# Kernel optimization log

Hardware: AMD Instinct MI355X
Metric: run time of the kernel (lower is better)

The kernel has to match this reference:

```python
import jax, jax.numpy as jnp
import numpy as np
import math

D_MODEL = 1024
NHEAD = 16
HEAD_DIM = D_MODEL // NHEAD
ROPE_BASE = 10000.0


def _rope(x):
    # x: [B, H, S, Dh]; rotate per the RoPE class (half-split variant)
    d = x.shape[-1]
    half = d // 2
    seq_len = x.shape[2]
    theta = 1.0 / (ROPE_BASE ** (jnp.arange(0, d, 2, dtype=jnp.float32) / d))  # [d/2]
    ang = jnp.arange(seq_len, dtype=jnp.float32)[:, None] * theta[None, :]      # [S, d/2]
    ang2 = jnp.concatenate([ang, ang], axis=-1)                                 # [S, d]
    cos_ = jnp.cos(ang2)[None, None, :, :]
    sin_ = jnp.sin(ang2)[None, None, :, :]
    neg_half = jnp.concatenate([-x[..., half:], x[..., :half]], axis=-1)
    return x * cos_ + neg_half * sin_


def setup_inputs() -> dict:
    key = jax.random.key(0)
    ks = jax.random.split(key, 10)
    B, S, D = 4, 2048, D_MODEL
    scale = 1.0 / math.sqrt(D)
    x = jax.random.normal(ks[0], (B, S, D), dtype=jnp.float32)
    Wq = jax.random.normal(ks[1], (D, D), dtype=jnp.float32) * scale
    bq = jnp.zeros((D,), dtype=jnp.float32)
    Wk = jax.random.normal(ks[2], (D, D), dtype=jnp.float32) * scale
    bk = jnp.zeros((D,), dtype=jnp.float32)
    Wv = jax.random.normal(ks[3], (D, D), dtype=jnp.float32) * scale
    bv = jnp.zeros((D,), dtype=jnp.float32)
    Wo = jax.random.normal(ks[4], (D, D), dtype=jnp.float32) * scale
    bo = jnp.zeros((D,), dtype=jnp.float32)
    # causal mask: mask==1 means masked (upper triangle)
    mask = jnp.triu(jnp.ones((S, S), dtype=jnp.int32), k=1)[None, None, :, :]
    return {"x": x, "Wq": Wq, "bq": bq, "Wk": Wk, "bk": bk,
            "Wv": Wv, "bv": bv, "Wo": Wo, "bo": bo, "mask": mask}


def reference(x, Wq, bq, Wk, bk, Wv, bv, Wo, bo, mask):
    B, S, D = x.shape
    H, Dh = NHEAD, HEAD_DIM

    def proj(W, b):
        y = jnp.einsum('bsd,ed->bse', x, W) + b  # torch Linear: x @ W.T + b
        return y.reshape(B, S, H, Dh).transpose(0, 2, 1, 3)  # [B,H,S,Dh]

    q = _rope(proj(Wq, bq))
    k = _rope(proj(Wk, bk))
    v = proj(Wv, bv)

    a = jnp.einsum('bhqd,bhkd->bhqk', q, k) / math.sqrt(Dh)  # [B,H,S,S]
    a = jnp.where(mask == 1, jnp.float32(-1e9), a)
    a = jax.nn.softmax(a, axis=-1)
    out = jnp.einsum('bhqk,bhkd->bhqd', a, v)                 # [B,H,S,Dh]
    out = out.transpose(0, 2, 1, 3).reshape(B, S, D)
    return jnp.einsum('bsd,ed->bse', out, Wo) + bo
```

## Files before the change

### kernel.cpp

```cpp
#include <hip/hip_runtime.h>
#include <stdint.h>

typedef unsigned short u16;
typedef __bf16 bf16x8 __attribute__((ext_vector_type(8)));
typedef __bf16 bf16x2 __attribute__((ext_vector_type(2)));
typedef float f32x4 __attribute__((ext_vector_type(4)));
typedef float f32x16 __attribute__((ext_vector_type(16)));

#define SEQ    2048
#define NHEAD  16
#define DH     64
#define DMODEL 1024
#define NBH    64

__device__ __forceinline__ u16 cvt1(float f){
  union { __bf16 h; u16 u; } c; c.h = (__bf16)f; return c.u;
}
__device__ __forceinline__ uint32_t cvt2(float a, float b){
  union { bf16x2 v; uint32_t u; } c; c.v = bf16x2{(__bf16)a, (__bf16)b}; return c.u;
}
__device__ __forceinline__ int swz(int row){ return (((row&7)^((row>>3)&7))<<4); }

#if __has_builtin(__builtin_amdgcn_exp2f)
__device__ __forceinline__ float EXP2(float x){ return __builtin_amdgcn_exp2f(x); }
#else
__device__ __forceinline__ float EXP2(float x){ return exp2f(x); }
#endif
__device__ __forceinline__ float max3f(float a, float b, float c){
  float r; asm("v_max3_f32 %0, %1, %2, %3" : "=v"(r) : "v"(a), "v"(b), "v"(c));
  return r;
}

typedef const __attribute__((address_space(1))) uint32_t* gas_t;
typedef __attribute__((address_space(3))) uint32_t* las_t;
__device__ __forceinline__ void async16(const void* g, void* l){
  __builtin_amdgcn_global_load_lds((gas_t)g, (las_t)l, 16, 0, 0);
}

__device__ __forceinline__ void vstore8(char* dst, uint2 a0, uint2 a1,
                                        uint2 b0, uint2 b1, int dc, int vpos){
  uint32_t pk[8];
  pk[0] = __builtin_amdgcn_perm(b0.x, a0.x, 0x05040100u);
  pk[1] = __builtin_amdgcn_perm(b0.x, a0.x, 0x07060302u);
  pk[2] = __builtin_amdgcn_perm(b0.y, a0.y, 0x05040100u);
  pk[3] = __builtin_amdgcn_perm(b0.y, a0.y, 0x07060302u);
  pk[4] = __builtin_amdgcn_perm(b1.x, a1.x, 0x05040100u);
  pk[5] = __builtin_amdgcn_perm(b1.x, a1.x, 0x07060302u);
  pk[6] = __builtin_amdgcn_perm(b1.y, a1.y, 0x05040100u);
  pk[7] = __builtin_amdgcn_perm(b1.y, a1.y, 0x07060302u);
#pragma unroll
  for (int e=0;e<8;e++){
    const int row = dc*8 + e;
    *(uint32_t*)(dst + ((row*128 + vpos*2) ^ swz(row))) = pk[e];
  }
}

__global__ void prep(const float* __restrict__ x,  const float* __restrict__ Wq,
                     const float* __restrict__ Wk, const float* __restrict__ Wv,
                     const float* __restrict__ Wo,
                     u16* __restrict__ xb, u16* __restrict__ wqkv,
                     u16* __restrict__ wob, float* __restrict__ tab)
{
  const int bid = blockIdx.x, tid = threadIdx.x;
  if (bid < 6144){
    const float* src; u16* dst; int lb;
    if      (bid < 4096){ src = x;  dst = xb;              lb = bid; }
    else if (bid < 4608){ src = Wq; dst = wqkv;            lb = bid-4096; }
    else if (bid < 5120){ src = Wk; dst = wqkv + 1048576;  lb = bid-4608; }
    else if (bid < 5632){ src = Wv; dst = wqkv + 2097152;  lb = bid-5120; }
    else                { src = Wo; dst = wob;             lb = bid-5632; }
    const size_t off = (size_t)lb*2048 + tid*8;
    float4 a = *(const float4*)(src+off);
    float4 b = *(const float4*)(src+off+4);
    bf16x8 o = { (__bf16)a.x,(__bf16)a.y,(__bf16)a.z,(__bf16)a.w,
                 (__bf16)b.x,(__bf16)b.y,(__bf16)b.z,(__bf16)b.w };
    *(bf16x8*)(dst+off) = o;
  } else {
    const int t = (bid-6144)*256 + tid;
    const int s = t >> 5, j = t & 31;
    double freq = exp(-(double)(2*j)/64.0*log(10000.0));
    double ang = (double)s*freq;
    tab[s*64 + 2*j]     = (float)cos(ang);
    tab[s*64 + 2*j + 1] = (float)sin(ang);
  }
}

template<int MODE>
__global__ __launch_bounds__(256, 2)
void gemm_bt(const u16* __restrict__ A, const u16* __restrict__ W,
             const float* __restrict__ b0, const float* __restrict__ b1,
             const float* __restrict__ b2, float* __restrict__ fout,
             u16* __restrict__ dq, u16* __restrict__ dk, u16* __restrict__ dv,
             const float* __restrict__ tab)
{
  __shared__ u16 Ab[2][128*64];
  __shared__ u16 Bb[2][128*64];
  const int tid = threadIdx.x;
  const int lane = tid & 63;
  const int w = tid >> 6, wr = w >> 1, wc = w & 1;
  const int id = blockIdx.x;
  const int bx = id >> 6;
  const int by = ((id & 7) << 3) | ((id >> 3) & 7);
  const int m0 = by * 128;
  const int n0 = bx * 128;
  const int c0 = lane & 15, g = lane >> 4;

  f32x4 acc[4][4] = {};

  const int srow = tid >> 3;
  const int gcol = (((tid & 7) ^ (srow & 7)) << 4);
  const char* ga = (const char*)A + (size_t)(m0 + srow)*2048 + gcol;
  const char* gb = (const char*)W + (size_t)(n0 + srow)*2048 + gcol;
  const int ldst = tid*16;

#define STAGE_G(buf, kbyte) do{ \
    _Pragma("unroll") \
    for (int k=0;k<4;k++){ \
      async16(ga + (kbyte) + k*32*2048, (char*)Ab[buf] + k*4096 + ldst); \
      async16(gb + (kbyte) + k*32*2048, (char*)Bb[buf] + k*4096 + ldst); \
    } \
  }while(0)

#define COMPUTE_G(buf) do{ \
    bf16x8 afr[2][4], bfr[2][4]; \
    _Pragma("unroll") \
    for (int kk=0;kk<2;kk++){ \
      _Pragma("unroll") \
      for (int i=0;i<4;i++){ \
        const int ra = wr*64 + i*16 + c0; \
        afr[kk][i] = *(const bf16x8*)((const char*)Ab[buf] + ra*128 + ((((kk*4+g) ^ (ra&7))) << 4)); \
        const int rb = wc*64 + i*16 + c0; \
        bfr[kk][i] = *(const bf16x8*)((const char*)Bb[buf] + rb*128 + ((((kk*4+g) ^ (rb&7))) << 4)); \
      } \
    } \
    __builtin_amdgcn_s_setprio(1); \
    _Pragma("unroll") \
    for (int kk=0;kk<2;kk++) \
      _Pragma("unroll") \
      for (int i=0;i<4;i++) \
        _Pragma("unroll") \
        for (int j=0;j<4;j++) \
          acc[i][j] = __builtin_amdgcn_mfma_f32_16x16x32_bf16(afr[kk][i], bfr[kk][j], acc[i][j], 0,0,0); \
    __builtin_amdgcn_s_setprio(0); \
  }while(0)

  STAGE_G(0, 0);
#pragma unroll 1
  for (int it = 0; it < 15; ++it) {
    const int cur = it & 1;
    STAGE_G(cur ^ 1, (it+1)*128);
    asm volatile("s_waitcnt vmcnt(8)" ::: "memory");
    __builtin_amdgcn_s_barrier();
    __builtin_amdgcn_sched_barrier(0);
    COMPUTE_G(cur);
    __builtin_amdgcn_s_barrier();
    __builtin_amdgcn_sched_barrier(0);
  }
  asm volatile("s_waitcnt vmcnt(0)" ::: "memory");
  __builtin_amdgcn_s_barrier();
  __builtin_amdgcn_sched_barrier(0);
  COMPUTE_G(1);
#undef STAGE_G
#undef COMPUTE_G

  const int nbase = n0 + wc*64;
  const int t = n0 >> 10;
  const float* bias = (MODE==1) ? b0 : (t==0) ? b0 : (t==1) ? b1 : b2;
  float bv4[4];
#pragma unroll
  for (int j=0;j<4;j++) bv4[j] = bias[(nbase & 1023) + j*16 + c0];

  if (MODE == 0) {
    u16* dst = (t==0) ? dq : (t==1) ? dk : dv;
    const float qs = (t==0) ? 0.18033688011f : 1.0f;
    const int h = (nbase >> 6) & (NHEAD-1);
#pragma unroll
    for (int i=0;i<4;i++){
      const int mbase = m0 + wr*64 + i*16 + g*4;
#pragma unroll
      for (int r=0;r<4;r++){
        const int mm = mbase + r;
        const int bb = mm >> 11, s = mm & (SEQ-1);
        const size_t rowbase = (((size_t)(bb*NHEAD + h))*SEQ + s)*DH;
        if (t < 2) {
#pragma unroll
          for (int j2=0;j2<2;j2++){
            const int dh = j2*16 + c0;
            const float xl = acc[i][j2][r]   + bv4[j2];
            const float xh = acc[i][j2+2][r] + bv4[j2+2];
            const float2 cs = *(const float2*)(tab + (size_t)s*64 + dh*2);
            dst[rowbase + dh]      = cvt1((xl*cs.x - xh*cs.y)*qs);
            dst[rowbase + dh + 32] = cvt1((xh*cs.x + xl*cs.y)*qs);
          }
        } else {
#pragma unroll
          for (int j=0;j<4;j++)
            dst[rowbase + j*16 + c0] = cvt1(acc[i][j][r] + bv4[j]);
        }
      }
    }
  } else {
#pragma unroll
    for (int i=0;i<4;i++){
      const int mbase = m0 + wr*64 + i*16 + g*4;
#pragma unroll
      for (int j=0;j<4;j++){
#pragma unroll
        for (int r=0;r<4;r++)
          fout[(size_t)(mbase + r) * DMODEL + nbase + j*16 + c0] = acc[i][j][r] + bv4[j];
      }
    }
  }
}

__global__ __launch_bounds__(256, 2)
void attn_fwd(const u16* __restrict__ Q, const u16* __restrict__ K,
              const u16* __restrict__ V, u16* __restrict__ O)
{
  __shared__ u16 Kb[2][64*64];
  __shared__ u16 Vt[2][64*64];
  const int bh = blockIdx.x;
  const int pair = blockIdx.y;
  const int tid = threadIdx.x, lane = tid & 63, w = tid >> 6;
  const int c31 = lane & 31, hi = lane >> 5;
  const size_t hb = (size_t)bh * SEQ * DH;
  const int b = bh >> 4, h = bh & 15;

  const int boff1 = tid*16;
  const int ksw1  = boff1 ^ swz(boff1 >> 7);
  const int boff2 = boff1 + 4096;
  const int ksw2  = boff2 ^ swz(boff2 >> 7);
  const int rp = tid >> 3, dc = tid & 7;
  const int kv0 = 2*rp;
  const int vpos = (kv0 & 0x33) | ((kv0 & 4) << 1) | ((kv0 & 8) >> 1);

#pragma unroll 1
  for (int half = 0; half < 2; half++){
    const int qt = half ? (15 - pair) : pair;
    const int qrow_base = qt*128 + w*32;
    const int jt_last  = 2*qt + 1;
    const int jt_end_w = 2*qt + (w>>1);
    const int q = qrow_base + c31;

    bf16x8 qf[4];
#pragma unroll
    for (int kc=0;kc<4;kc++)
      qf[kc] = *(const bf16x8*)(Q + hb + (size_t)q*DH + kc*16 + hi*8);

    f32x16 oacc0 = {}, oacc1 = {};
    float mrun = -3.0e38f, lrun = 0.f;

    uint2 pa0, pa1, pb0, pb1;

    {
      const u16* gv = V + hb;
      pa0 = *(const uint2*)(gv + (kv0  )*DH + dc*8);
      pa1 = *(const uint2*)(gv + (kv0  )*DH + dc*8 + 4);
      pb0 = *(const uint2*)(gv + (kv0+1)*DH + dc*8);
      pb1 = *(const uint2*)(gv + (kv0+1)*DH + dc*8 + 4);
      __builtin_amdgcn_sched_barrier(0);
      const char* gk = (const char*)(K + hb);
      async16(gk + ksw1, (char*)Kb[0] + boff1);
      async16(gk + ksw2, (char*)Kb[0] + boff2);
      vstore8((char*)Vt[0], pa0, pa1, pb0, pb1, dc, vpos);
    }
    __syncthreads();

    for (int jt = 0; jt <= jt_last; jt++){
      const int cur = jt & 1, nxt = cur ^ 1;
      const bool pre = (jt < jt_last);
      if (pre){
        const u16* gv = V + hb + (size_t)(jt+1)*64*DH;
        pa0 = *(const uint2*)(gv + (kv0  )*DH + dc*8);
        pa1 = *(const uint2*)(gv + (kv0  )*DH + dc*8 + 4);
        pb0 = *(const uint2*)(gv + (kv0+1)*DH + dc*8);
        pb1 = *(const uint2*)(gv + (kv0+1)*DH + dc*8 + 4);
        __builtin_amdgcn_sched_barrier(0);
        const char* gk = (const char*)(K + hb + (size_t)(jt+1)*64*DH);
        async16(gk + ksw1, (char*)Kb[nxt] + boff1);
        async16(gk + ksw2, (char*)Kb[nxt] + boff2);
      }

      if (jt <= jt_end_w){
        if (pre) asm volatile("s_waitcnt vmcnt(6)" ::: "memory");
        else     asm volatile("s_waitcnt vmcnt(0)" ::: "memory");
        f32x16 sT[2] = {};
#pragma unroll
        for (int kc=0;kc<4;kc++){
          const int col = (kc*16 + hi*8)*2;
          const int r0 = c31, r1 = 32 + c31;
          const bf16x8 kf0 = *(const bf16x8*)((const char*)Kb[cur] + ((r0*128 + col) ^ swz(r0)));
          const bf16x8 kf1 = *(const bf16x8*)((const char*)Kb[cur] + ((r1*128 + col) ^ swz(r1)));
          __builtin_amdgcn_s_setprio(1);
          sT[0] = __builtin_amdgcn_mfma_f32_32x32x16_bf16(kf0, qf[kc], sT[0], 0,0,0);
          sT[1] = __builtin_amdgcn_mfma_f32_32x32x16_bf16(kf1, qf[kc], sT[1], 0,0,0);
          __builtin_amdgcn_s_setprio(0);
        }
        if (jt == jt_end_w){
#pragma unroll
          for (int kvb=0;kvb<2;kvb++)
#pragma unroll
            for (int r=0;r<16;r++){
              const int kv = jt*64 + kvb*32 + (r&3) + 8*(r>>2) + 4*hi;
              sT[kvb][r] = (kv <= q) ? sT[kvb][r] : -3.0e38f;
            }
        }
        float mx0 = -3.0e38f, mx1 = -3.0e38f;
#pragma unroll
        for (int r=0;r<16;r+=2){
          mx0 = max3f(mx0, sT[0][r], sT[0][r+1]);
          mx1 = max3f(mx1, sT[1][r], sT[1][r+1]);
        }
        float mx = fmaxf(mx0, mx1);
        mx = fmaxf(mx, __shfl_xor(mx, 32));
        const bool grow = __any(mx > mrun + 8.0f);
        float corr = 1.0f;
        if (grow){
          const float mnew = fmaxf(mrun, mx);
          corr = EXP2(mrun - mnew);
          mrun = mnew;
        }
        float ls[4] = {0.f, 0.f, 0.f, 0.f};
#pragma unroll
        for (int kvb=0;kvb<2;kvb++)
#pragma unroll
          for (int r=0;r<16;r++){
            const float p = EXP2(sT[kvb][r] - mrun);
            sT[kvb][r] = p;
            ls[r & 3] += p;
          }
        float lsum = (ls[0] + ls[1]) + (ls[2] + ls[3]);
        lsum += __shfl_xor(lsum, 32);
        lrun = lrun*corr + lsum;
        if (grow){
#pragma unroll
          for (int r=0;r<16;r++){ oacc0[r] *= corr; oacc1[r] *= corr; }
        }
#pragma unroll
        for (int kvb=0;kvb<2;kvb++)
#pragma unroll
          for (int s=0;s<2;s++){
            union { bf16x8 v; uint32_t d[4]; } pa;
#pragma unroll
            for (int j=0;j<4;j++)
              pa.d[j] = cvt2(sT[kvb][s*8+2*j], sT[kvb][s*8+2*j+1]);
            const int col = (kvb*32 + s*16 + hi*8)*2;
            const int r0 = c31, r1 = 32 + c31;
            const bf16x8 vf0 = *(const bf16x8*)((const char*)Vt[cur] + ((r0*128 + col) ^ swz(r0)));
            const bf16x8 vf1 = *(const bf16x8*)((const char*)Vt[cur] + ((r1*128 + col) ^ swz(r1)));
            __builtin_amdgcn_s_setprio(1);
            oacc0 = __builtin_amdgcn_mfma_f32_32x32x16_bf16(vf0, pa.v, oacc0, 0,0,0);
            oacc1 = __builtin_amdgcn_mfma_f32_32x32x16_bf16(vf1, pa.v, oacc1, 0,0,0);
            __builtin_amdgcn_s_setprio(0);
          }
      }

      if (pre){
        asm volatile("s_waitcnt vmcnt(2)" ::: "memory");
        vstore8((char*)Vt[nxt], pa0, pa1, pb0, pb1, dc, vpos);
      }
      asm volatile("s_waitcnt lgkmcnt(0)" ::: "memory");
      __builtin_amdgcn_s_barrier();
      __builtin_amdgcn_sched_barrier(0);
    }

    {
      const float inv = 1.0f / lrun;
      u16* orow = O + ((size_t)b*SEQ + q)*DMODEL + h*DH;
#pragma unroll
      for (int r2=0;r2<8;r2++){
        const int dh0 = 2*(r2&1) + 8*(r2>>1) + 4*hi;
        *(uint32_t*)(orow + dh0)      = cvt2(oacc0[2*r2]*inv, oacc0[2*r2+1]*inv);
        *(uint32_t*)(orow + 32 + dh0) = cvt2(oacc1[2*r2]*inv, oacc1[2*r2+1]*inv);
      }
    }
  }
}

extern "C" void kernel_launch(void* const* d_in, const int* in_sizes, int n_in,
                              void* d_out, int out_size, void* d_ws, size_t ws_size,
                              hipStream_t stream)
{
  const float* x  = (const float*)d_in[0];
  const float* Wq = (const float*)d_in[1];
  const float* bq = (const float*)d_in[2];
  const float* Wk = (const float*)d_in[3];
  const float* bk = (const float*)d_in[4];
  const float* Wv = (const float*)d_in[5];
  const float* bv = (const float*)d_in[6];
  const float* Wo = (const float*)d_in[7];
  const float* bo = (const float*)d_in[8];

  const size_t MB = 1024*1024;
  char* ws = (char*)d_ws;
  u16*  xb   = (u16*)(ws);
  u16*  aw   = (u16*)(ws);
  u16*  vw   = (u16*)(ws + 16*MB);
  u16*  wqkv = (u16*)(ws + 32*MB);
  u16*  wob  = (u16*)(ws + 38*MB);
  float* tab = (float*)(ws + 41*MB);
  u16*  qw = (u16*)d_out;
  u16*  kw = (u16*)d_out + 8*MB;

  prep<<<dim3(6400), dim3(256), 0, stream>>>(x, Wq, Wk, Wv, Wo, xb, wqkv, wob, tab);

  gemm_bt<0><<<dim3(1536), dim3(256), 0, stream>>>(xb, wqkv, bq, bk, bv,
                                                   nullptr, qw, kw, vw, tab);

  attn_fwd<<<dim3(64, 8), dim3(256), 0, stream>>>(qw, kw, vw, aw);

  gemm_bt<1><<<dim3(512), dim3(256), 0, stream>>>(aw, wob, bo, nullptr, nullptr,
                                                  (float*)d_out, nullptr, nullptr, nullptr, nullptr);
}
```

Measured before the change: 163.0 us.

## Use 256x128 tiles with K=32 stages for the QKV projection GEMM

The QKV GEMM becomes its own kernel that uses 256x128 output tiles, with each wave computing 128x64, and a 32-wide K step double-buffered in LDS. The grid drops from 1536 to 768 blocks. Bigger tiles raise arithmetic intensity and cut redundant global reads of the weight matrix. In exchange the accumulators double to 128 registers per thread, which may hurt occupancy, and there are twice as many barrier-synchronised K iterations. The output projection keeps the old tiling as a separate specialised kernel.

```diff
diff --git a/kernel.cpp b/kernel.cpp
--- a/kernel.cpp
+++ b/kernel.cpp
@@ -85,13 +85,119 @@
   }
 }
 
-template<int MODE>
 __global__ __launch_bounds__(256, 2)
-void gemm_bt(const u16* __restrict__ A, const u16* __restrict__ W,
-             const float* __restrict__ b0, const float* __restrict__ b1,
-             const float* __restrict__ b2, float* __restrict__ fout,
-             u16* __restrict__ dq, u16* __restrict__ dk, u16* __restrict__ dv,
-             const float* __restrict__ tab)
+void gemm_qkv(const u16* __restrict__ A, const u16* __restrict__ W,
+              const float* __restrict__ b0, const float* __restrict__ b1,
+              const float* __restrict__ b2,
+              u16* __restrict__ dq, u16* __restrict__ dk, u16* __restrict__ dv,
+              const float* __restrict__ tab)
+{
+  __shared__ u16 Ab[2][256*32];
+  __shared__ u16 Bb[2][128*32];
+  const int tid = threadIdx.x, lane = tid & 63;
+  const int w = tid >> 6, wm = w >> 1, wn = w & 1;
+  const int c0 = lane & 15, g = lane >> 4;
+  const int id = blockIdx.x;
+  const int by = (id & 7)*4 + ((id >> 3) & 3);
+  const int bx = id >> 5;
+  const int m0 = by * 256, n0 = bx * 128;
+
+  f32x4 acc[8][4] = {};
+
+  const int srow = tid >> 2;
+  const int gcol = (((tid & 3) ^ (srow & 3)) << 4);
+  const char* ga = (const char*)A + (size_t)(m0 + srow)*2048 + gcol;
+  const char* gb = (const char*)W + (size_t)(n0 + srow)*2048 + gcol;
+  const int ldst = tid*16;
+
+#define STAGE_Q(buf, kbyte) do{ \
+    _Pragma("unroll") \
+    for (int k=0;k<4;k++) \
+      async16(ga + (kbyte) + k*64*2048, (char*)Ab[buf] + k*4096 + ldst); \
+    _Pragma("unroll") \
+    for (int k=0;k<2;k++) \
+      async16(gb + (kbyte) + k*64*2048, (char*)Bb[buf] + k*4096 + ldst); \
+  }while(0)
+
+#define COMPUTE_Q(buf) do{ \
+    bf16x8 bfr[4], afr[8]; \
+    _Pragma("unroll") \
+    for (int j=0;j<4;j++){ \
+      const int rb = wn*64 + j*16 + c0; \
+      bfr[j] = *(const bf16x8*)((const char*)Bb[buf] + rb*64 + (((g ^ (rb&3))) << 4)); \
+    } \
+    _Pragma("unroll") \
+    for (int i=0;i<8;i++){ \
+      const int ra = wm*128 + i*16 + c0; \
+      afr[i] = *(const bf16x8*)((const char*)Ab[buf] + ra*64 + (((g ^ (ra&3))) << 4)); \
+    } \
+    __builtin_amdgcn_s_setprio(1); \
+    _Pragma("unroll") \
+    for (int i=0;i<8;i++) \
+      _Pragma("unroll") \
+      for (int j=0;j<4;j++) \
+        acc[i][j] = __builtin_amdgcn_mfma_f32_16x16x32_bf16(afr[i], bfr[j], acc[i][j], 0,0,0); \
+    __builtin_amdgcn_s_setprio(0); \
+  }while(0)
+
+  STAGE_Q(0, 0);
+#pragma unroll 1
+  for (int it = 0; it < 31; ++it) {
+    const int cur = it & 1;
+    STAGE_Q(cur ^ 1, (it+1)*64);
+    asm volatile("s_waitcnt vmcnt(6)" ::: "memory");
+    __builtin_amdgcn_s_barrier();
+    __builtin_amdgcn_sched_barrier(0);
+    COMPUTE_Q(cur);
+    __builtin_amdgcn_s_barrier();
+    __builtin_amdgcn_sched_barrier(0);
+  }
+  asm volatile("s_waitcnt vmcnt(0)" ::: "memory");
+  __builtin_amdgcn_s_barrier();
+  __builtin_amdgcn_sched_barrier(0);
+  COMPUTE_Q(1);
+#undef STAGE_Q
+#undef COMPUTE_Q
+
+  const int nbase = n0 + wn*64;
+  const int tsel = n0 >> 10;
+  const float* bias = (tsel==0) ? b0 : (tsel==1) ? b1 : b2;
+  float bv4[4];
+#pragma unroll
+  for (int j=0;j<4;j++) bv4[j] = bias[(nbase & 1023) + j*16 + c0];
+  u16* dst = (tsel==0) ? dq : (tsel==1) ? dk : dv;
+  const float qs = (tsel==0) ? 0.18033688011f : 1.0f;
+  const int h = (nbase >> 6) & (NHEAD-1);
+#pragma unroll
+  for (int i=0;i<8;i++){
+    const int mbase = m0 + wm*128 + i*16 + g*4;
+#pragma unroll
+    for (int r=0;r<4;r++){
+      const int mm = mbase + r;
+      const int bb = mm >> 11, s = mm & (SEQ-1);
+      const size_t rowbase = (((size_t)(bb*NHEAD + h))*SEQ + s)*DH;
+      if (tsel < 2){
+#pragma unroll
+        for (int j2=0;j2<2;j2++){
+          const int dh = j2*16 + c0;
+          const float xl = acc[i][j2][r]   + bv4[j2];
+          const float xh = acc[i][j2+2][r] + bv4[j2+2];
+          const float2 cs = *(const float2*)(tab + (size_t)s*64 + dh*2);
+          dst[rowbase + dh]      = cvt1((xl*cs.x - xh*cs.y)*qs);
+          dst[rowbase + dh + 32] = cvt1((xh*cs.x + xl*cs.y)*qs);
+        }
+      } else {
+#pragma unroll
+        for (int j=0;j<4;j++)
+          dst[rowbase + j*16 + c0] = cvt1(acc[i][j][r] + bv4[j]);
+      }
+    }
+  }
+}
+
+__global__ __launch_bounds__(256, 2)
+void gemm_o(const u16* __restrict__ A, const u16* __restrict__ W,
+            const float* __restrict__ b0, float* __restrict__ fout)
 {
   __shared__ u16 Ab[2][128*64];
   __shared__ u16 Bb[2][128*64];
@@ -113,7 +219,7 @@
   const char* gb = (const char*)W + (size_t)(n0 + srow)*2048 + gcol;
   const int ldst = tid*16;
 
-#define STAGE_G(buf, kbyte) do{ \
+#define STAGE_O(buf, kbyte) do{ \
     _Pragma("unroll") \
     for (int k=0;k<4;k++){ \
       async16(ga + (kbyte) + k*32*2048, (char*)Ab[buf] + k*4096 + ldst); \
@@ -121,7 +227,7 @@
     } \
   }while(0)
 
-#define COMPUTE_G(buf) do{ \
+#define COMPUTE_O(buf) do{ \
     bf16x8 afr[2][4], bfr[2][4]; \
     _Pragma("unroll") \
     for (int kk=0;kk<2;kk++){ \
@@ -144,71 +250,37 @@
     __builtin_amdgcn_s_setprio(0); \
   }while(0)
 
-  STAGE_G(0, 0);
+  STAGE_O(0, 0);
 #pragma unroll 1
   for (int it = 0; it < 15; ++it) {
     const int cur = it & 1;
-    STAGE_G(cur ^ 1, (it+1)*128);
+    STAGE_O(cur ^ 1, (it+1)*128);
     asm volatile("s_waitcnt vmcnt(8)" ::: "memory");
     __builtin_amdgcn_s_barrier();
     __builtin_amdgcn_sched_barrier(0);
-    COMPUTE_G(cur);
+    COMPUTE_O(cur);
     __builtin_amdgcn_s_barrier();
     __builtin_amdgcn_sched_barrier(0);
   }
   asm volatile("s_waitcnt vmcnt(0)" ::: "memory");
   __builtin_amdgcn_s_barrier();
   __builtin_amdgcn_sched_barrier(0);
-  COMPUTE_G(1);
-#undef STAGE_G
-#undef COMPUTE_G
+  COMPUTE_O(1);
+#undef STAGE_O
+#undef COMPUTE_O
 
   const int nbase = n0 + wc*64;
-  const int t = n0 >> 10;
-  const float* bias = (MODE==1) ? b0 : (t==0) ? b0 : (t==1) ? b1 : b2;
   float bv4[4];
 #pragma unroll
-  for (int j=0;j<4;j++) bv4[j] = bias[(nbase & 1023) + j*16 + c0];
-
-  if (MODE == 0) {
-    u16* dst = (t==0) ? dq : (t==1) ? dk : dv;
-    const float qs = (t==0) ? 0.18033688011f : 1.0f;
-    const int h = (nbase >> 6) & (NHEAD-1);
-#pragma unroll
-    for (int i=0;i<4;i++){
-      const int mbase = m0 + wr*64 + i*16 + g*4;
-#pragma unroll
-      for (int r=0;r<4;r++){
-        const int mm = mbase + r;
-        const int bb = mm >> 11, s = mm & (SEQ-1);
-        const size_t rowbase = (((size_t)(bb*NHEAD + h))*SEQ + s)*DH;
-        if (t < 2) {
-#pragma unroll
-          for (int j2=0;j2<2;j2++){
-            const int dh = j2*16 + c0;
-            const float xl = acc[i][j2][r]   + bv4[j2];
-            const float xh = acc[i][j2+2][r] + bv4[j2+2];
-            const float2 cs = *(const float2*)(tab + (size_t)s*64 + dh*2);
-            dst[rowbase + dh]      = cvt1((xl*cs.x - xh*cs.y)*qs);
-            dst[rowbase + dh + 32] = cvt1((xh*cs.x + xl*cs.y)*qs);
-          }
-        } else {
-#pragma unroll
-          for (int j=0;j<4;j++)
-            dst[rowbase + j*16 + c0] = cvt1(acc[i][j][r] + bv4[j]);
-        }
-      }
-    }
-  } else {
-#pragma unroll
-    for (int i=0;i<4;i++){
-      const int mbase = m0 + wr*64 + i*16 + g*4;
-#pragma unroll
-      for (int j=0;j<4;j++){
-#pragma unroll
-        for (int r=0;r<4;r++)
-          fout[(size_t)(mbase + r) * DMODEL + nbase + j*16 + c0] = acc[i][j][r] + bv4[j];
-      }
+  for (int j=0;j<4;j++) bv4[j] = b0[(nbase & 1023) + j*16 + c0];
+#pragma unroll
+  for (int i=0;i<4;i++){
+    const int mbase = m0 + wr*64 + i*16 + g*4;
+#pragma unroll
+    for (int j=0;j<4;j++){
+#pragma unroll
+      for (int r=0;r<4;r++)
+        fout[(size_t)(mbase + r) * DMODEL + nbase + j*16 + c0] = acc[i][j][r] + bv4[j];
     }
   }
 }
@@ -404,11 +476,10 @@
 
   prep<<<dim3(6400), dim3(256), 0, stream>>>(x, Wq, Wk, Wv, Wo, xb, wqkv, wob, tab);
 
-  gemm_bt<0><<<dim3(1536), dim3(256), 0, stream>>>(xb, wqkv, bq, bk, bv,
-                                                   nullptr, qw, kw, vw, tab);
+  gemm_qkv<<<dim3(768), dim3(256), 0, stream>>>(xb, wqkv, bq, bk, bv,
+                                                qw, kw, vw, tab);
 
   attn_fwd<<<dim3(64, 8), dim3(256), 0, stream>>>(qw, kw, vw, aw);
 
-  gemm_bt<1><<<dim3(512), dim3(256), 0, stream>>>(aw, wob, bo, nullptr, nullptr,
-                                                  (float*)d_out, nullptr, nullptr, nullptr, nullptr);
-}
+  gemm_o<<<dim3(512), dim3(256), 0, stream>>>(aw, wob, bo, (float*)d_out);
+}
```

Result: slower. 176.7 us (+8.4%).

## Enlarge attention KV tile from 64 to 128 rows per iteration

Applied to the files above, without the earlier changes.

The attention kernel now processes 128 keys per loop iteration instead of 64. It double-buffers larger K and V-transpose tiles in LDS and computes four 32-row score blocks per warp. This halves the number of barriers and loop iterations per query tile, and issues more independent MFMAs between syncs. In exchange it doubles LDS use and raises register pressure. It also drops the per-warp early exit on the diagonal, so every warp computes the full masked last tile.

```diff
diff --git a/kernel.cpp b/kernel.cpp
--- a/kernel.cpp
+++ b/kernel.cpp
@@ -37,8 +37,8 @@
   __builtin_amdgcn_global_load_lds((gas_t)g, (las_t)l, 16, 0, 0);
 }
 
-__device__ __forceinline__ void vstore8(char* dst, uint2 a0, uint2 a1,
-                                        uint2 b0, uint2 b1, int dc, int vpos){
+__device__ __forceinline__ void vstore8w(char* dst, uint2 a0, uint2 a1,
+                                         uint2 b0, uint2 b1, int dc, int vpos){
   uint32_t pk[8];
   pk[0] = __builtin_amdgcn_perm(b0.x, a0.x, 0x05040100u);
   pk[1] = __builtin_amdgcn_perm(b0.x, a0.x, 0x07060302u);
@@ -51,7 +51,7 @@
 #pragma unroll
   for (int e=0;e<8;e++){
     const int row = dc*8 + e;
-    *(uint32_t*)(dst + ((row*128 + vpos*2) ^ swz(row))) = pk[e];
+    *(uint32_t*)(dst + ((row*256 + vpos*2) ^ swz(row))) = pk[e];
   }
 }
 
@@ -217,8 +217,8 @@
 void attn_fwd(const u16* __restrict__ Q, const u16* __restrict__ K,
               const u16* __restrict__ V, u16* __restrict__ O)
 {
-  __shared__ u16 Kb[2][64*64];
-  __shared__ u16 Vt[2][64*64];
+  __shared__ u16 Kb[2][128*64];
+  __shared__ u16 Vt[2][64*128];
   const int bh = blockIdx.x;
   const int pair = blockIdx.y;
   const int tid = threadIdx.x, lane = tid & 63, w = tid >> 6;
@@ -226,10 +226,13 @@
   const size_t hb = (size_t)bh * SEQ * DH;
   const int b = bh >> 4, h = bh & 15;
 
-  const int boff1 = tid*16;
-  const int ksw1  = boff1 ^ swz(boff1 >> 7);
-  const int boff2 = boff1 + 4096;
-  const int ksw2  = boff2 ^ swz(boff2 >> 7);
+  const int boff = tid*16;
+  int ksw[4];
+#pragma unroll
+  for (int k2=0;k2<4;k2++){
+    const int off = boff + k2*4096;
+    ksw[k2] = off ^ swz(off >> 7);
+  }
   const int rp = tid >> 3, dc = tid & 7;
   const int kv0 = 2*rp;
   const int vpos = (kv0 & 0x33) | ((kv0 & 4) << 1) | ((kv0 & 8) >> 1);
@@ -238,8 +241,7 @@
   for (int half = 0; half < 2; half++){
     const int qt = half ? (15 - pair) : pair;
     const int qrow_base = qt*128 + w*32;
-    const int jt_last  = 2*qt + 1;
-    const int jt_end_w = 2*qt + (w>>1);
+    const int jt_last = qt;
     const int q = qrow_base + c31;
 
     bf16x8 qf[4];
@@ -251,18 +253,25 @@
     float mrun = -3.0e38f, lrun = 0.f;
 
     uint2 pa0, pa1, pb0, pb1;
+    uint2 qa0, qa1, qb0, qb1;
 
     {
       const u16* gv = V + hb;
-      pa0 = *(const uint2*)(gv + (kv0  )*DH + dc*8);
-      pa1 = *(const uint2*)(gv + (kv0  )*DH + dc*8 + 4);
-      pb0 = *(const uint2*)(gv + (kv0+1)*DH + dc*8);
-      pb1 = *(const uint2*)(gv + (kv0+1)*DH + dc*8 + 4);
+      pa0 = *(const uint2*)(gv + (kv0     )*DH + dc*8);
+      pa1 = *(const uint2*)(gv + (kv0     )*DH + dc*8 + 4);
+      pb0 = *(const uint2*)(gv + (kv0 +  1)*DH + dc*8);
+      pb1 = *(const uint2*)(gv + (kv0 +  1)*DH + dc*8 + 4);
+      qa0 = *(const uint2*)(gv + (kv0 + 64)*DH + dc*8);
+      qa1 = *(const uint2*)(gv + (kv0 + 64)*DH + dc*8 + 4);
+      qb0 = *(const uint2*)(gv + (kv0 + 65)*DH + dc*8);
+      qb1 = *(const uint2*)(gv + (kv0 + 65)*DH + dc*8 + 4);
       __builtin_amdgcn_sched_barrier(0);
       const char* gk = (const char*)(K + hb);
-      async16(gk + ksw1, (char*)Kb[0] + boff1);
-      async16(gk + ksw2, (char*)Kb[0] + boff2);
-      vstore8((char*)Vt[0], pa0, pa1, pb0, pb1, dc, vpos);
+#pragma unroll
+      for (int k2=0;k2<4;k2++)
+        async16(gk + ksw[k2], (char*)Kb[0] + boff + k2*4096);
+      vstore8w((char*)Vt[0], pa0, pa1, pb0, pb1, dc, vpos);
+      vstore8w((char*)Vt[0], qa0, qa1, qb0, qb1, dc, vpos + 64);
     }
     __syncthreads();
 
@@ -270,94 +279,104 @@
       const int cur = jt & 1, nxt = cur ^ 1;
       const bool pre = (jt < jt_last);
       if (pre){
-        const u16* gv = V + hb + (size_t)(jt+1)*64*DH;
-        pa0 = *(const uint2*)(gv + (kv0  )*DH + dc*8);
-        pa1 = *(const uint2*)(gv + (kv0  )*DH + dc*8 + 4);
-        pb0 = *(const uint2*)(gv + (kv0+1)*DH + dc*8);
-        pb1 = *(const uint2*)(gv + (kv0+1)*DH + dc*8 + 4);
+        const u16* gv = V + hb + (size_t)(jt+1)*128*DH;
+        pa0 = *(const uint2*)(gv + (kv0     )*DH + dc*8);
+        pa1 = *(const uint2*)(gv + (kv0     )*DH + dc*8 + 4);
+        pb0 = *(const uint2*)(gv + (kv0 +  1)*DH + dc*8);
+        pb1 = *(const uint2*)(gv + (kv0 +  1)*DH + dc*8 + 4);
+        qa0 = *(const uint2*)(gv + (kv0 + 64)*DH + dc*8);
+        qa1 = *(const uint2*)(gv + (kv0 + 64)*DH + dc*8 + 4);
+        qb0 = *(const uint2*)(gv + (kv0 + 65)*DH + dc*8);
+        qb1 = *(const uint2*)(gv + (kv0 + 65)*DH + dc*8 + 4);
         __builtin_amdgcn_sched_barrier(0);
-        const char* gk = (const char*)(K + hb + (size_t)(jt+1)*64*DH);
-        async16(gk + ksw1, (char*)Kb[nxt] + boff1);
-        async16(gk + ksw2, (char*)Kb[nxt] + boff2);
-      }
-
-      if (jt <= jt_end_w){
-        if (pre) asm volatile("s_waitcnt vmcnt(6)" ::: "memory");
-        else     asm volatile("s_waitcnt vmcnt(0)" ::: "memory");
-        f32x16 sT[2] = {};
-#pragma unroll
-        for (int kc=0;kc<4;kc++){
-          const int col = (kc*16 + hi*8)*2;
+        const char* gk = (const char*)(K + hb + (size_t)(jt+1)*128*DH);
+#pragma unroll
+        for (int k2=0;k2<4;k2++)
+          async16(gk + ksw[k2], (char*)Kb[nxt] + boff + k2*4096);
+      }
+
+      if (pre) asm volatile("s_waitcnt vmcnt(12)" ::: "memory");
+      else     asm volatile("s_waitcnt vmcnt(0)" ::: "memory");
+
+      f32x16 sT[4] = {};
+#pragma unroll
+      for (int kc=0;kc<4;kc++){
+        const int col = (kc*16 + hi*8)*2;
+        bf16x8 kf[4];
+#pragma unroll
+        for (int kvb=0;kvb<4;kvb++){
+          const int rr = kvb*32 + c31;
+          kf[kvb] = *(const bf16x8*)((const char*)Kb[cur] + ((rr*128 + col) ^ swz(rr)));
+        }
+        __builtin_amdgcn_s_setprio(1);
+#pragma unroll
+        for (int kvb=0;kvb<4;kvb++)
+          sT[kvb] = __builtin_amdgcn_mfma_f32_32x32x16_bf16(kf[kvb], qf[kc], sT[kvb], 0,0,0);
+        __builtin_amdgcn_s_setprio(0);
+      }
+      if (jt == jt_last){
+#pragma unroll
+        for (int kvb=0;kvb<4;kvb++)
+#pragma unroll
+          for (int r=0;r<16;r++){
+            const int kv = jt*128 + kvb*32 + (r&3) + 8*(r>>2) + 4*hi;
+            sT[kvb][r] = (kv <= q) ? sT[kvb][r] : -3.0e38f;
+          }
+      }
+      float mxc[4] = {-3.0e38f,-3.0e38f,-3.0e38f,-3.0e38f};
+#pragma unroll
+      for (int r=0;r<16;r+=2){
+#pragma unroll
+        for (int kvb=0;kvb<4;kvb++)
+          mxc[kvb] = max3f(mxc[kvb], sT[kvb][r], sT[kvb][r+1]);
+      }
+      float mx = fmaxf(fmaxf(mxc[0], mxc[1]), fmaxf(mxc[2], mxc[3]));
+      mx = fmaxf(mx, __shfl_xor(mx, 32));
+      const bool grow = __any(mx > mrun + 8.0f);
+      float corr = 1.0f;
+      if (grow){
+        const float mnew = fmaxf(mrun, mx);
+        corr = EXP2(mrun - mnew);
+        mrun = mnew;
+      }
+      float ls[4] = {0.f, 0.f, 0.f, 0.f};
+#pragma unroll
+      for (int kvb=0;kvb<4;kvb++)
+#pragma unroll
+        for (int r=0;r<16;r++){
+          const float p = EXP2(sT[kvb][r] - mrun);
+          sT[kvb][r] = p;
+          ls[r & 3] += p;
+        }
+      float lsum = (ls[0] + ls[1]) + (ls[2] + ls[3]);
+      lsum += __shfl_xor(lsum, 32);
+      lrun = lrun*corr + lsum;
+      if (grow){
+#pragma unroll
+        for (int r=0;r<16;r++){ oacc0[r] *= corr; oacc1[r] *= corr; }
+      }
+#pragma unroll
+      for (int kvb=0;kvb<4;kvb++)
+#pragma unroll
+        for (int s=0;s<2;s++){
+          union { bf16x8 v; uint32_t d[4]; } pa;
+#pragma unroll
+          for (int j=0;j<4;j++)
+            pa.d[j] = cvt2(sT[kvb][s*8+2*j], sT[kvb][s*8+2*j+1]);
+          const int col = (kvb*32 + s*16 + hi*8)*2;
           const int r0 = c31, r1 = 32 + c31;
-          const bf16x8 kf0 = *(const bf16x8*)((const char*)Kb[cur] + ((r0*128 + col) ^ swz(r0)));
-          const bf16x8 kf1 = *(const bf16x8*)((const char*)Kb[cur] + ((r1*128 + col) ^ swz(r1)));
+          const bf16x8 vf0 = *(const bf16x8*)((const char*)Vt[cur] + ((r0*256 + col) ^ swz(r0)));
+          const bf16x8 vf1 = *(const bf16x8*)((const char*)Vt[cur] + ((r1*256 + col) ^ swz(r1)));
           __builtin_amdgcn_s_setprio(1);
-          sT[0] = __builtin_amdgcn_mfma_f32_32x32x16_bf16(kf0, qf[kc], sT[0], 0,0,0);
-          sT[1] = __builtin_amdgcn_mfma_f32_32x32x16_bf16(kf1, qf[kc], sT[1], 0,0,0);
+          oacc0 = __builtin_amdgcn_mfma_f32_32x32x16_bf16(vf0, pa.v, oacc0, 0,0,0);
+          oacc1 = __builtin_amdgcn_mfma_f32_32x32x16_bf16(vf1, pa.v, oacc1, 0,0,0);
           __builtin_amdgcn_s_setprio(0);
         }
-        if (jt == jt_end_w){
-#pragma unroll
-          for (int kvb=0;kvb<2;kvb++)
-#pragma unroll
-            for (int r=0;r<16;r++){
-              const int kv = jt*64 + kvb*32 + (r&3) + 8*(r>>2) + 4*hi;
-              sT[kvb][r] = (kv <= q) ? sT[kvb][r] : -3.0e38f;
-            }
-        }
-        float mx0 = -3.0e38f, mx1 = -3.0e38f;
-#pragma unroll
-        for (int r=0;r<16;r+=2){
-          mx0 = max3f(mx0, sT[0][r], sT[0][r+1]);
-          mx1 = max3f(mx1, sT[1][r], sT[1][r+1]);
-        }
-        float mx = fmaxf(mx0, mx1);
-        mx = fmaxf(mx, __shfl_xor(mx, 32));
-        const bool grow = __any(mx > mrun + 8.0f);
-        float corr = 1.0f;
-        if (grow){
-          const float mnew = fmaxf(mrun, mx);
-          corr = EXP2(mrun - mnew);
-          mrun = mnew;
-        }
-        float ls[4] = {0.f, 0.f, 0.f, 0.f};
-#pragma unroll
-        for (int kvb=0;kvb<2;kvb++)
-#pragma unroll
-          for (int r=0;r<16;r++){
-            const float p = EXP2(sT[kvb][r] - mrun);
-            sT[kvb][r] = p;
-            ls[r & 3] += p;
-          }
-        float lsum = (ls[0] + ls[1]) + (ls[2] + ls[3]);
-        lsum += __shfl_xor(lsum, 32);
-        lrun = lrun*corr + lsum;
-        if (grow){
-#pragma unroll
-          for (int r=0;r<16;r++){ oacc0[r] *= corr; oacc1[r] *= corr; }
-        }
-#pragma unroll
-        for (int kvb=0;kvb<2;kvb++)
-#pragma unroll
-          for (int s=0;s<2;s++){
-            union { bf16x8 v; uint32_t d[4]; } pa;
-#pragma unroll
-            for (int j=0;j<4;j++)
-              pa.d[j] = cvt2(sT[kvb][s*8+2*j], sT[kvb][s*8+2*j+1]);
-            const int col = (kvb*32 + s*16 + hi*8)*2;
-            const int r0 = c31, r1 = 32 + c31;
-            const bf16x8 vf0 = *(const bf16x8*)((const char*)Vt[cur] + ((r0*128 + col) ^ swz(r0)));
-            const bf16x8 vf1 = *(const bf16x8*)((const char*)Vt[cur] + ((r1*128 + col) ^ swz(r1)));
-            __builtin_amdgcn_s_setprio(1);
-            oacc0 = __builtin_amdgcn_mfma_f32_32x32x16_bf16(vf0, pa.v, oacc0, 0,0,0);
-            oacc1 = __builtin_amdgcn_mfma_f32_32x32x16_bf16(vf1, pa.v, oacc1, 0,0,0);
-            __builtin_amdgcn_s_setprio(0);
-          }
-      }
 
       if (pre){
-        asm volatile("s_waitcnt vmcnt(2)" ::: "memory");
-        vstore8((char*)Vt[nxt], pa0, pa1, pb0, pb1, dc, vpos);
+        asm volatile("s_waitcnt vmcnt(4)" ::: "memory");
+        vstore8w((char*)Vt[nxt], pa0, pa1, pb0, pb1, dc, vpos);
+        vstore8w((char*)Vt[nxt], qa0, qa1, qb0, qb1, dc, vpos + 64);
       }
       asm volatile("s_waitcnt lgkmcnt(0)" ::: "memory");
       __builtin_amdgcn_s_barrier();
```

Result: no change. 164.9 us (+1.2%).
